# Optimization experiments

Measured on AMD Instinct MI355X. Metric: run time of the kernel, lower is better.

Reference implementation:

```python
import jax, jax.numpy as jnp
import numpy as np

IN_CH = 512; OUT_CH = 512; NOISE_SIZE = 512; K = 3; A = 0.2
B = 4; H = 32
_G = float(np.sqrt(2.0 / (1.0 + A * A)))                 # leaky_relu gain, a=0.2
CONV_SCALE = _G / float(np.sqrt(IN_CH * K * K))          # equal-lr kaiming scale (fan_in = in_ch*3*3)
MS_SCALE = float(np.sqrt(2.0 / (NOISE_SIZE + IN_CH)))    # equal-lr xavier scale on make_s linear
RGB_SCALE = _G * float(np.sqrt(2.0 / (OUT_CH + 3)))      # equal-lr xavier scale on 1x1 to_rgb


def upsample2x(x):
    # torch F.interpolate(scale_factor=2, mode='bilinear', align_corners=False)
    b, c, h, w = x.shape
    return jax.image.resize(x, (b, c, 2 * h, 2 * w), method='bilinear')


def mod_conv(x, style, weight, bias, ms_w, ms_b, w_scale, demodulate, pad):
    # style -> per-sample input-channel scales s: (B, Cin)
    s = style @ (ms_w.T * MS_SCALE) + ms_b
    Wmod = (weight * w_scale)[None] * s[:, None, :, None, None]   # (B, Cout, Cin, k, k)
    if demodulate:
        d = jax.lax.rsqrt(jnp.sum(Wmod * Wmod, axis=(2, 3, 4)) + 1e-8)
        Wmod = Wmod * d[:, :, None, None, None]
    conv1 = lambda xi, wi: jax.lax.conv_general_dilated(
        xi[None], wi, (1, 1), [(pad, pad), (pad, pad)],
        dimension_numbers=('NCHW', 'OIHW', 'NCHW'))[0]
    y = jax.vmap(conv1)(x, Wmod)                                   # per-sample weights == grouped conv
    return y + bias[None, :, None, None]


def lrelu(x):
    return jnp.where(x >= 0, x, A * x)


def setup_inputs() -> dict:
    key = jax.random.key(0)
    ks = jax.random.split(key, 19)
    r = lambda i, shape: jax.random.normal(ks[i], shape, dtype=jnp.float32)
    return {
        'maps': r(0, (B, IN_CH, H, H)),
        'w': r(1, (B, NOISE_SIZE)),
        'rgb': r(2, (B, 3, H, H)),
        'noise0': r(3, (B, 1, 2 * H, 2 * H)),
        'noise1': r(4, (B, 1, 2 * H, 2 * H)),
        'conv0_w': r(5, (OUT_CH, IN_CH, K, K)),
        'conv0_b': 0.1 * r(6, (OUT_CH,)),
        'ms0_w': r(7, (IN_CH, NOISE_SIZE)),
        'ms0_b': jnp.ones((IN_CH,), jnp.float32),
        'ns0': 0.1 * r(8, (OUT_CH,)),
        'conv1_w': r(9, (OUT_CH, OUT_CH, K, K)),
        'conv1_b': 0.1 * r(10, (OUT_CH,)),
        'ms1_w': r(11, (OUT_CH, NOISE_SIZE)),
        'ms1_b': jnp.ones((OUT_CH,), jnp.float32),
        'ns1': 0.1 * r(12, (OUT_CH,)),
        'rgb_w': r(13, (3, OUT_CH, 1, 1)),
        'rgb_b': 0.1 * r(14, (3,)),
        'msr_w': r(15, (OUT_CH, NOISE_SIZE)),
        'msr_b': jnp.ones((OUT_CH,), jnp.float32),
    }


def reference(maps, w, rgb, noise0, noise1,
              conv0_w, conv0_b, ms0_w, ms0_b, ns0,
              conv1_w, conv1_b, ms1_w, ms1_b, ns1,
              rgb_w, rgb_b, msr_w, msr_b):
    # upsample branch (upsample=True)
    rgb = upsample2x(rgb)
    maps = upsample2x(maps)
    # layer 0: modulated conv -> noise -> leaky relu
    h = mod_conv(maps, w, conv0_w, conv0_b, ms0_w, ms0_b, CONV_SCALE, True, 1)
    h = lrelu(h + ns0[None, :, None, None] * noise0)
    # layer 1
    h = mod_conv(h, w, conv1_w, conv1_b, ms1_w, ms1_b, CONV_SCALE, True, 1)
    h = lrelu(h + ns1[None, :, None, None] * noise1)
    # to_rgb: 1x1 modulated conv, no demodulation
    rgb_out = rgb + mod_conv(h, w, rgb_w, rgb_b, msr_w, msr_b, RGB_SCALE, False, 0)
    return (rgb_out, h)
```

## Files before the change

### kernel.cpp

```cpp
#include <hip/hip_runtime.h>
#include <stdint.h>


#define BATCH 4
#define CH 512
#define NPP 4356
#define HOUT_OFF 49152

static constexpr double G_GAIN = 1.3867504905630728;
static constexpr float CONV_SCALE_F = (float)(G_GAIN / 67.88225099390857);
static constexpr float MS_SCALE_F = 0.044194173824159216f;
static constexpr float RGB_SCALE_F = (float)(G_GAIN * 1.4142135623730951 / 22.693611435820433);

typedef __attribute__((ext_vector_type(8))) short short8;
typedef __attribute__((ext_vector_type(4))) float floatx4;

#define OFF_S0     256
#define OFF_S1     (OFF_S0 + 8192)
#define OFF_SR     (OFF_S1 + 8192)
#define OFF_D0     (OFF_SR + 8192)
#define OFF_D1     (OFF_D0 + 8192)
#define OFF_B0F    (OFF_D1 + 8192)
#define OFF_B1F    (OFF_B0F + 2048)
#define OFF_NS0F   (OFF_B1F + 2048)
#define OFF_NS1F   (OFF_NS0F + 2048)
#define OFF_WMODR  (OFF_NS1F + 2048)
#define OFF_N0F    (OFF_WMODR + 24576)
#define OFF_N1F    (OFF_N0F + 65536)
#define OFF_WT0    (OFF_N1F + 65536)
#define WT_BYTES   4718592
#define OFF_WT1    (OFF_WT0 + WT_BYTES)
#define OFF_XP0    (OFF_WT1 + WT_BYTES)
#define XP_BYTES   17842176
#define OFF_XP1    (OFF_XP0 + XP_BYTES)

__device__ __forceinline__ float bf2f(unsigned short u) {
  return __uint_as_float(((unsigned int)u) << 16);
}
__device__ __forceinline__ unsigned short f2bf(float f) {
  unsigned int x = __float_as_uint(f);
  unsigned int r = x + 0x7FFFu + ((x >> 16) & 1u);
  return (unsigned short)(r >> 16);
}
__device__ __forceinline__ float ldin(const void* p, long i, int bf) {
  if (bf) return bf2f(((const unsigned short*)p)[i]);
  return ((const float*)p)[i];
}
__device__ __forceinline__ int bfflag_of(const void* msb) {
  return ((const unsigned int*)msb)[0] == 0x3F803F80u ? 1 : 0;
}
__device__ __forceinline__ void async_ld16(const void* g, void* l) {
  __builtin_amdgcn_global_load_lds(
      (const __attribute__((address_space(1))) unsigned int*)g,
      (__attribute__((address_space(3))) unsigned int*)l, 16, 0, 0);
}
__device__ __forceinline__ void upw(int o, int n_in, int& lo, int& hi, float& wlo) {
  int k = o >> 1;
  if (o & 1) { lo = k; hi = k + 1; if (hi > n_in - 1) hi = n_in - 1; wlo = 0.75f; }
  else       { lo = k - 1; if (lo < 0) lo = 0; hi = k; wlo = 0.25f; }
}

__global__ void k_pre(const void* w, const void* msw0, const void* msb0,
                      const void* msw1, const void* msb1,
                      const void* mswr, const void* msbr,
                      const void* b0, const void* b1, const void* nv0,
                      const void* nv1, const void* noise0, const void* noise1,
                      float* s0, float* s1, float* sr,
                      float* ob0, float* ob1, float* ons0, float* ons1,
                      float* on0, float* on1, unsigned short* Xp) {
  const int bf = bfflag_of(msb0);
  const int bid = blockIdx.x;
  if (bid < 264) {
    const int idx = bid * 256 + threadIdx.x;
    const int plane = idx / 132;
    const int rem = idx - plane * 132;
    const int row65 = rem >= 66;
    const int col = rem - (row65 ? 66 : 0);
    const short8 z = {0, 0, 0, 0, 0, 0, 0, 0};
    *(short8*)&Xp[((long)plane * NPP + (row65 ? 65 : 0) * 66 + col) * 8] = z;
    return;
  }
  if (bid < 648) {
    const int b2 = bid - 264;
    const int mat = b2 >> 7, chunk = b2 & 127;
    const int wv = threadIdx.x >> 6, lane = threadIdx.x & 63;
    const int i = chunk * 4 + wv;
    const void* msw; const void* msb; float* out;
    if (mat == 0)      { msw = msw0; msb = msb0; out = s0; }
    else if (mat == 1) { msw = msw1; msb = msb1; out = s1; }
    else               { msw = mswr; msb = msbr; out = sr; }
    float a[4] = {0.f, 0.f, 0.f, 0.f};
    const int n0 = lane * 8;
    if (bf) {
      short8 m8 = *(const short8*)((const unsigned short*)msw + (long)i * 512 + n0);
      for (int b = 0; b < 4; ++b) {
        short8 w8 = *(const short8*)((const unsigned short*)w + b * 512 + n0);
        float s = 0.f;
        for (int e = 0; e < 8; ++e)
          s += bf2f((unsigned short)m8[e]) * bf2f((unsigned short)w8[e]);
        a[b] = s;
      }
    } else {
      const float* mrow = (const float*)msw + (long)i * 512 + n0;
      float4 m0v = *(const float4*)mrow, m1v = *(const float4*)(mrow + 4);
      for (int b = 0; b < 4; ++b) {
        const float* wr = (const float*)w + b * 512 + n0;
        float4 w0v = *(const float4*)wr, w1v = *(const float4*)(wr + 4);
        a[b] = m0v.x * w0v.x + m0v.y * w0v.y + m0v.z * w0v.z + m0v.w * w0v.w +
               m1v.x * w1v.x + m1v.y * w1v.y + m1v.z * w1v.z + m1v.w * w1v.w;
      }
    }
    for (int off = 1; off < 64; off <<= 1)
      for (int b = 0; b < 4; ++b) a[b] += __shfl_xor(a[b], off, 64);
    if (lane == 0) {
      const float mb = ldin(msb, i, bf);
      for (int b = 0; b < 4; ++b) out[b * 512 + i] = a[b] * MS_SCALE_F + mb;
    }
    return;
  }
  const int t = (bid - 648) * 256 + threadIdx.x;
  if (t < 512) {
    ob0[t] = ldin(b0, t, bf); ob1[t] = ldin(b1, t, bf);
    ons0[t] = ldin(nv0, t, bf); ons1[t] = ldin(nv1, t, bf);
  }
  on0[t] = ldin(noise0, t, bf);
  on1[t] = ldin(noise1, t, bf);
}

__global__ void k_mid(const void* w0, const void* w1,
                      const float* s0, const float* s1, const float* sr,
                      const void* rw, unsigned short* Wt0, unsigned short* Wt1,
                      float* S0, float* S1, float* owmr,
                      const void* maps, unsigned short* Xp0, const void* msb) {
  const int bf = bfflag_of(msb);
  const int bid = blockIdx.x;
  __shared__ float smem[32 * 4 * 32];
  if (bid < 256) {
    const int l = bid >> 7, cog = bid & 127;
    const void* w = l ? w1 : w0;
    const float* s = l ? s1 : s0;
    unsigned short* Wt = l ? Wt1 : Wt0;
    float* S = l ? S1 : S0;
    const int co_sub = threadIdx.x >> 6;
    const int kb = (threadIdx.x >> 2) & 15, q = threadIdx.x & 3;
    const int co = cog * 4 + co_sub;
    const int ci0 = kb * 32 + q * 8;
    const long base = ((long)co * 512 + ci0) * 9;
    float v[9][8];
    if (bf) {
      const unsigned short* wp = (const unsigned short*)w + base;
      short8 r[9];
#pragma unroll
      for (int k = 0; k < 9; ++k) r[k] = *(const short8*)(wp + k * 8);
#pragma unroll
      for (int j = 0; j < 8; ++j)
#pragma unroll
        for (int t = 0; t < 9; ++t) {
          const int off = j * 9 + t;
          v[t][j] = bf2f((unsigned short)r[off >> 3][off & 7]);
        }
    } else {
      const float* wp = (const float*)w + base;
      float4 r[18];
#pragma unroll
      for (int k = 0; k < 18; ++k) r[k] = *(const float4*)(wp + k * 4);
#pragma unroll
      for (int j = 0; j < 8; ++j)
#pragma unroll
        for (int t = 0; t < 9; ++t) {
          const int off = j * 9 + t;
          const float4 rr = r[off >> 2];
          const int c2 = off & 3;
          v[t][j] = c2 == 0 ? rr.x : (c2 == 1 ? rr.y : (c2 == 2 ? rr.z : rr.w));
        }
    }
#pragma unroll
    for (int t = 0; t < 9; ++t) {
      short8 pk;
#pragma unroll
      for (int j = 0; j < 8; ++j) pk[j] = (short)f2bf(v[t][j]);
      *(short8*)&Wt[((long)(t * 16 + kb) * 4 + q) * 4096 + co * 8] = pk;
    }
    float wsq[8];
#pragma unroll
    for (int j = 0; j < 8; ++j) {
      float a = 0.f;
#pragma unroll
      for (int t = 0; t < 9; ++t) a += v[t][j] * v[t][j];
      wsq[j] = a;
    }
    float part[4];
#pragma unroll
    for (int b4 = 0; b4 < 4; ++b4) {
      const float* sp = s + b4 * 512 + ci0;
      float4 sa = *(const float4*)sp, sb = *(const float4*)(sp + 4);
      part[b4] = sa.x * sa.x * wsq[0] + sa.y * sa.y * wsq[1] +
                 sa.z * sa.z * wsq[2] + sa.w * sa.w * wsq[3] +
                 sb.x * sb.x * wsq[4] + sb.y * sb.y * wsq[5] +
                 sb.z * sb.z * wsq[6] + sb.w * sb.w * wsq[7];
    }
    for (int off = 1; off < 64; off <<= 1)
#pragma unroll
      for (int b4 = 0; b4 < 4; ++b4)
        part[b4] += __shfl_xor(part[b4], off, 64);
    if ((threadIdx.x & 63) == 0)
#pragma unroll
      for (int b4 = 0; b4 < 4; ++b4) S[b4 * 512 + co] = part[b4];
    return;
  }
  if (bid < 1280) {
    const int bid2 = bid - 256;
    const int t = bid2 & 15, kb = (bid2 >> 4) & 15, b = bid2 >> 8;
    float (*lds)[4][32] = (float(*)[4][32])smem;
    {
      const int ciq = threadIdx.x >> 5;
      const int x = threadIdx.x & 31;
      for (int cc = 0; cc < 4; ++cc) {
        const int ci = cc * 8 + ciq;
        const long cbase = ((long)(b * 512 + kb * 32 + ci)) << 10;
        for (int r = 0; r < 4; ++r) {
          int ir = 2 * t - 1 + r;
          ir = ir < 0 ? 0 : (ir > 31 ? 31 : ir);
          lds[ci][r][x] = ldin(maps, cbase + ir * 32 + x, bf);
        }
      }
    }
    __syncthreads();
    const int q = threadIdx.x >> 6, px = threadIdx.x & 63;
    int xlo, xhi; float wx;
    upw(px, 32, xlo, xhi, wx);
    float sv[8];
    for (int jj = 0; jj < 8; ++jj) sv[jj] = s0[b * 512 + kb * 32 + q * 8 + jj];
    for (int y = 0; y < 4; ++y) {
      const int yg = 4 * t + y;
      int ylo, yhi; float wy;
      upw(yg, 32, ylo, yhi, wy);
      const int rlo = ylo - (2 * t - 1), rhi = yhi - (2 * t - 1);
      short8 pk;
      for (int jj = 0; jj < 8; ++jj) {
        const int ci = q * 8 + jj;
        float vlo = wx * lds[ci][rlo][xlo] + (1.f - wx) * lds[ci][rlo][xhi];
        float vhi = wx * lds[ci][rhi][xlo] + (1.f - wx) * lds[ci][rhi][xhi];
        float v = (wy * vlo + (1.f - wy) * vhi) * sv[jj];
        pk[jj] = (short)f2bf(v);
      }
      *(short8*)&Xp0[((((long)b * 16 + kb) * 4 + q) * NPP + (yg + 1) * 66 + (px + 1)) * 8] = pk;
    }
    return;
  }
  const int i = (bid - 1280) * 256 + threadIdx.x;
  const int b = i / 1536; const int r = i - b * 1536;
  const int c = r >> 9; const int ci = r & 511;
  owmr[i] = RGB_SCALE_F * ldin(rw, c * 512 + ci, bf) * sr[b * 512 + ci];
}

#define MFMA16 __builtin_amdgcn_mfma_f32_16x16x32_bf16
template <int LAYER>
__global__ __launch_bounds__(512, 2) void k_conv(
    const unsigned short* __restrict__ Wt,
    const unsigned short* Xp,
    const float* __restrict__ Ssum,
    const float* __restrict__ bias,
    const float* __restrict__ nsc,
    const float* __restrict__ noise,
    const float* __restrict__ snext,
    unsigned short* XpOut,
    void* dout,
    const void* __restrict__ msb) {
  __shared__ __align__(16) unsigned short AB[49152];
  const int idx = blockIdx.x;
  const int mt = idx & 3, b = (idx >> 2) & 3, nt = idx >> 4;
  const int m0 = mt << 7, y0 = nt << 2;
  const int lane = threadIdx.x & 63, wv = threadIdx.x >> 6;
  const int wm = wv >> 2, wn = wv & 3;
  const int q = lane >> 4, l15 = lane & 15;

  const floatx4 vz = {0.f, 0.f, 0.f, 0.f};
  floatx4 c00 = vz, c01 = vz, c02 = vz, c03 = vz;
  floatx4 c10 = vz, c11 = vz, c12 = vz, c13 = vz;
  floatx4 c20 = vz, c21 = vz, c22 = vz, c23 = vz;
  floatx4 c30 = vz, c31 = vz, c32 = vz, c33 = vz;

  const int vA = (q << 10) + (wm << 9) + (l15 << 3);
  const int BB = 24576;
  const int vB   = (q << 9) + (l15 << 3);
  const int vBm1 = (q << 9) + ((l15 == 0 ? 0 : l15 - 1) << 3);
  const int vBp1 = (q << 9) + ((l15 == 15 ? 15 : l15 + 1) << 3);
  const bool e0 = (l15 == 0), e15 = (l15 == 15);

  auto issueB6 = [&](int kbn, int half) {
#pragma unroll
    for (int k = 0; k < 3; ++k) {
      const int t = wv * 3 + k;
      const int row = t >> 2, qq = t & 3;
      const unsigned short* src =
          Xp + ((((long)b * 16 + kbn) * 4 + qq) * NPP + (long)(y0 + row) * 66 + 1 + lane) * 8;
      async_ld16(src, &AB[BB + half * 12288 + ((row * 4 + qq) << 9)]);
    }
  };
  auto issueA = [&](int kb, int ky, int par) {
#pragma unroll
    for (int k = 0; k < 3; ++k) {
      const int c = wv * 3 + k;
      const int half64 = c & 1, chunk = c >> 1;
      const int kx = chunk >> 2, qq = chunk & 3;
      const unsigned short* src =
          Wt + ((long)(((ky * 3 + kx) * 16 + kb) * 4 + qq) << 12) +
          ((m0 + half64 * 64 + lane) << 3);
      async_ld16(src, &AB[par * 12288 + chunk * 1024 + half64 * 512]);
    }
  };

  const short8 z8 = {0, 0, 0, 0, 0, 0, 0, 0};

#define RND(KY, PA, HB, KB, NKB, NKY, NPA, DOB, DKB, DHB)                      \
  {                                                                            \
    __syncthreads();                                                           \
    issueA((NKB), (NKY), (NPA));                                               \
    if (DOB) issueB6((DKB), (DHB));                                            \
    const int ab = (PA) * 12288 + vA;                                          \
    short8 a00 = *(const short8*)&AB[ab];                                      \
    short8 a01 = *(const short8*)&AB[ab + 128];                                \
    short8 a02 = *(const short8*)&AB[ab + 256];                                \
    short8 a03 = *(const short8*)&AB[ab + 384];                                \
    short8 a10 = *(const short8*)&AB[ab + 4096];                               \
    short8 a11 = *(const short8*)&AB[ab + 4224];                               \
    short8 a12 = *(const short8*)&AB[ab + 4352];                               \
    short8 a13 = *(const short8*)&AB[ab + 4480];                               \
    short8 a20 = *(const short8*)&AB[ab + 8192];                               \
    short8 a21 = *(const short8*)&AB[ab + 8320];                               \
    short8 a22 = *(const short8*)&AB[ab + 8448];                               \
    short8 a23 = *(const short8*)&AB[ab + 8576];                               \
    const int bo = BB + (HB) * 12288 + ((wn + (KY)) << 11);                    \
    {                                                              \
      short8 b0 = *(const short8*)&AB[vBm1 + bo];                              \
      short8 b1 = *(const short8*)&AB[vB + bo + 120];                          \
      short8 b2 = *(const short8*)&AB[vB + bo + 248];                          \
      short8 b3 = *(const short8*)&AB[vB + bo + 376];                          \
      b0 = e0 ? z8 : b0;                                                       \
      c00 = MFMA16(a00, b0, c00, 0, 0, 0); c01 = MFMA16(a00, b1, c01, 0, 0, 0);\
      c02 = MFMA16(a00, b2, c02, 0, 0, 0); c03 = MFMA16(a00, b3, c03, 0, 0, 0);\
      c10 = MFMA16(a01, b0, c10, 0, 0, 0); c11 = MFMA16(a01, b1, c11, 0, 0, 0);\
      c12 = MFMA16(a01, b2, c12, 0, 0, 0); c13 = MFMA16(a01, b3, c13, 0, 0, 0);\
      c20 = MFMA16(a02, b0, c20, 0, 0, 0); c21 = MFMA16(a02, b1, c21, 0, 0, 0);\
      c22 = MFMA16(a02, b2, c22, 0, 0, 0); c23 = MFMA16(a02, b3, c23, 0, 0, 0);\
      c30 = MFMA16(a03, b0, c30, 0, 0, 0); c31 = MFMA16(a03, b1, c31, 0, 0, 0);\
      c32 = MFMA16(a03, b2, c32, 0, 0, 0); c33 = MFMA16(a03, b3, c33, 0, 0, 0);\
    }                                                                          \
    {                                                              \
      short8 b0 = *(const short8*)&AB[vB + bo];                                \
      short8 b1 = *(const short8*)&AB[vB + bo + 128];                          \
      short8 b2 = *(const short8*)&AB[vB + bo + 256];                          \
      short8 b3 = *(const short8*)&AB[vB + bo + 384];                          \
      c00 = MFMA16(a10, b0, c00, 0, 0, 0); c01 = MFMA16(a10, b1, c01, 0, 0, 0);\
      c02 = MFMA16(a10, b2, c02, 0, 0, 0); c03 = MFMA16(a10, b3, c03, 0, 0, 0);\
      c10 = MFMA16(a11, b0, c10, 0, 0, 0); c11 = MFMA16(a11, b1, c11, 0, 0, 0);\
      c12 = MFMA16(a11, b2, c12, 0, 0, 0); c13 = MFMA16(a11, b3, c13, 0, 0, 0);\
      c20 = MFMA16(a12, b0, c20, 0, 0, 0); c21 = MFMA16(a12, b1, c21, 0, 0, 0);\
      c22 = MFMA16(a12, b2, c22, 0, 0, 0); c23 = MFMA16(a12, b3, c23, 0, 0, 0);\
      c30 = MFMA16(a13, b0, c30, 0, 0, 0); c31 = MFMA16(a13, b1, c31, 0, 0, 0);\
      c32 = MFMA16(a13, b2, c32, 0, 0, 0); c33 = MFMA16(a13, b3, c33, 0, 0, 0);\
    }                                                                          \
    {                                                              \
      short8 b0 = *(const short8*)&AB[vB + bo + 8];                            \
      short8 b1 = *(const short8*)&AB[vB + bo + 136];                          \
      short8 b2 = *(const short8*)&AB[vB + bo + 264];                          \
      short8 b3 = *(const short8*)&AB[vBp1 + bo + 384];                        \
      b3 = e15 ? z8 : b3;                                                      \
      c00 = MFMA16(a20, b0, c00, 0, 0, 0); c01 = MFMA16(a20, b1, c01, 0, 0, 0);\
      c02 = MFMA16(a20, b2, c02, 0, 0, 0); c03 = MFMA16(a20, b3, c03, 0, 0, 0);\
      c10 = MFMA16(a21, b0, c10, 0, 0, 0); c11 = MFMA16(a21, b1, c11, 0, 0, 0);\
      c12 = MFMA16(a21, b2, c12, 0, 0, 0); c13 = MFMA16(a21, b3, c13, 0, 0, 0);\
      c20 = MFMA16(a22, b0, c20, 0, 0, 0); c21 = MFMA16(a22, b1, c21, 0, 0, 0);\
      c22 = MFMA16(a22, b2, c22, 0, 0, 0); c23 = MFMA16(a22, b3, c23, 0, 0, 0);\
      c30 = MFMA16(a23, b0, c30, 0, 0, 0); c31 = MFMA16(a23, b1, c31, 0, 0, 0);\
      c32 = MFMA16(a23, b2, c32, 0, 0, 0); c33 = MFMA16(a23, b3, c33, 0, 0, 0);\
    }                                                                          \
  }

  issueA(0, 0, 0);
  issueB6(0, 0);

#pragma unroll 1
  for (int it = 0; it < 8; ++it) {
    const int kb = it * 2, kb1 = kb + 1, kb2 = (kb + 2) & 15;
    RND(0, 0, 0, kb,  kb,  1, 1, 1, kb1, 1)
    RND(1, 1, 0, kb,  kb,  2, 0, 0, 0,  0)
    RND(2, 0, 0, kb,  kb1, 0, 1, 0, 0,  0)
    RND(0, 1, 1, kb1, kb1, 1, 0, 1, kb2, 0)
    RND(1, 0, 1, kb1, kb1, 2, 1, 0, 0,  0)
    RND(2, 1, 1, kb1, kb2, 0, 0, 0, 0,  0)
  }
#undef RND

  floatx4 accv[4][4] = {{c00, c01, c02, c03}, {c10, c11, c12, c13},
                        {c20, c21, c22, c23}, {c30, c31, c32, c33}};
  const int bfflag = bfflag_of(msb);
  const int coB = m0 + (wm << 6) + ((lane >> 4) << 2);
  const int xB = lane & 15;
  const int y = y0 + wn;
  for (int i = 0; i < 4; ++i) {
    const int co = coB + (i << 4);
    float Ds[4], bi[4], nv[4], sx[4];
    for (int r = 0; r < 4; ++r) {
      float Sv = Ssum[b * 512 + co + r];
      Ds[r] = CONV_SCALE_F * rsqrtf(CONV_SCALE_F * CONV_SCALE_F * Sv + 1e-8f);
      bi[r] = bias[co + r];
      nv[r] = nsc[co + r];
      sx[r] = (LAYER == 0) ? snext[b * 512 + co + r] : 0.f;
    }
    for (int j = 0; j < 4; ++j) {
      const int x = (j << 4) + xB;
      const int p = (y << 6) + x;
      const float nz = noise[b * 4096 + p];
      if (LAYER == 0) {
        unsigned long long pk = 0ull;
        for (int r = 0; r < 4; ++r) {
          float v = accv[i][j][r] * Ds[r] + bi[r] + nv[r] * nz;
          v = (v >= 0.f) ? v : 0.2f * v;
          pk |= (unsigned long long)f2bf(v * sx[r]) << (16 * r);
        }
        const int pp = (y + 1) * 66 + (x + 1);
        const long o = ((((long)b * 16 + (co >> 5)) * 4 + ((co >> 3) & 3)) * NPP + pp) * 8 + (co & 7);
        *(unsigned long long*)(XpOut + o) = pk;
      } else {
        for (int r = 0; r < 4; ++r) {
          float v = accv[i][j][r] * Ds[r] + bi[r] + nv[r] * nz;
          v = (v >= 0.f) ? v : 0.2f * v;
          const long o = (((long)(b * 512 + co + r)) << 12) + p;
          if (bfflag) ((unsigned short*)dout)[HOUT_OFF + o] = f2bf(v);
          else        ((float*)dout)[HOUT_OFF + o] = v;
        }
      }
    }
  }
}

__global__ void k_rgb(const void* rgb_in, const float* wmodr, const void* rb,
                      void* dout, const void* msb) {
  const int bf = bfflag_of(msb);
  const int b = blockIdx.y, p0 = blockIdx.x * 512;
  const int g = threadIdx.x >> 6, lane = threadIdx.x & 63;
  const int px = p0 + lane * 8;
  const char* hbytes = (const char*)dout + (long)HOUT_OFF * (bf ? 2 : 4);
  const float* wm = wmodr + b * 1536;
  float a0[8] = {}, a1[8] = {}, a2[8] = {};
  for (int ci = g * 128; ci < g * 128 + 128; ++ci) {
    const long o = (((long)(b * 512 + ci)) << 12) + px;
    float hv[8];
    if (bf) {
      short8 h8 = *(const short8*)((const unsigned short*)hbytes + o);
#pragma unroll
      for (int k = 0; k < 8; ++k) hv[k] = bf2f((unsigned short)h8[k]);
    } else {
      float4 f0 = *(const float4*)((const float*)hbytes + o);
      float4 f1 = *(const float4*)((const float*)hbytes + o + 4);
      hv[0] = f0.x; hv[1] = f0.y; hv[2] = f0.z; hv[3] = f0.w;
      hv[4] = f1.x; hv[5] = f1.y; hv[6] = f1.z; hv[7] = f1.w;
    }
    const float w0 = wm[ci], w1 = wm[512 + ci], w2 = wm[1024 + ci];
#pragma unroll
    for (int k = 0; k < 8; ++k) {
      a0[k] += w0 * hv[k]; a1[k] += w1 * hv[k]; a2[k] += w2 * hv[k];
    }
  }
  __shared__ float red[4][3][512];
#pragma unroll
  for (int k = 0; k < 8; ++k) {
    red[g][0][lane * 8 + k] = a0[k];
    red[g][1][lane * 8 + k] = a1[k];
    red[g][2][lane * 8 + k] = a2[k];
  }
  __syncthreads();
  for (int e = 0; e < 2; ++e) {
    const int pp = threadIdx.x * 2 + e;
    const int p = p0 + pp;
    const int y = p >> 6, x = p & 63;
    int ylo, yhi, xlo, xhi; float wy, wx;
    upw(y, 32, ylo, yhi, wy);
    upw(x, 32, xlo, xhi, wx);
    for (int c = 0; c < 3; ++c) {
      float s = red[0][c][pp] + red[1][c][pp] + red[2][c][pp] + red[3][c][pp];
      const long base = (long)(b * 3 + c) << 10;
      const float v00 = ldin(rgb_in, base + ylo * 32 + xlo, bf);
      const float v01 = ldin(rgb_in, base + ylo * 32 + xhi, bf);
      const float v10 = ldin(rgb_in, base + yhi * 32 + xlo, bf);
      const float v11 = ldin(rgb_in, base + yhi * 32 + xhi, bf);
      const float up = wy * (wx * v00 + (1.f - wx) * v01) +
                       (1.f - wy) * (wx * v10 + (1.f - wx) * v11);
      const float v = up + s + ldin(rb, c, bf);
      const long o = ((long)(b * 3 + c) << 12) + p;
      if (bf) ((unsigned short*)dout)[o] = f2bf(v);
      else    ((float*)dout)[o] = v;
    }
  }
}

extern "C" void kernel_launch(void* const* d_in, const int* in_sizes, int n_in,
                              void* d_out, int out_size, void* d_ws, size_t ws_size,
                              hipStream_t stream) {
  char* ws = (char*)d_ws;
  float* s0 = (float*)(ws + OFF_S0);
  float* s1 = (float*)(ws + OFF_S1);
  float* sr = (float*)(ws + OFF_SR);
  float* S0 = (float*)(ws + OFF_D0);
  float* S1 = (float*)(ws + OFF_D1);
  float* b0f = (float*)(ws + OFF_B0F);
  float* b1f = (float*)(ws + OFF_B1F);
  float* ns0f = (float*)(ws + OFF_NS0F);
  float* ns1f = (float*)(ws + OFF_NS1F);
  float* wmodr = (float*)(ws + OFF_WMODR);
  float* n0f = (float*)(ws + OFF_N0F);
  float* n1f = (float*)(ws + OFF_N1F);
  unsigned short* Wt0 = (unsigned short*)(ws + OFF_WT0);
  unsigned short* Wt1 = (unsigned short*)(ws + OFF_WT1);
  unsigned short* Xp0 = (unsigned short*)(ws + OFF_XP0);
  unsigned short* Xp1 = (unsigned short*)(ws + OFF_XP1);

  k_pre<<<712, 256, 0, stream>>>(d_in[1], d_in[7], d_in[8], d_in[12], d_in[13],
                                 d_in[17], d_in[18], d_in[6], d_in[11], d_in[9],
                                 d_in[14], d_in[3], d_in[4],
                                 s0, s1, sr, b0f, b1f, ns0f, ns1f, n0f, n1f, Xp0);
  k_mid<<<1304, 256, 0, stream>>>(d_in[5], d_in[10], s0, s1, sr, d_in[15],
                                  Wt0, Wt1, S0, S1, wmodr, d_in[0], Xp0, d_in[8]);
  k_conv<0><<<256, 512, 0, stream>>>(Wt0, Xp0, S0, b0f, ns0f, n0f, s1, Xp1,
                                     d_out, d_in[8]);
  k_conv<1><<<256, 512, 0, stream>>>(Wt1, Xp1, S1, b1f, ns1f, n1f, s1, Xp1,
                                     d_out, d_in[8]);
  k_rgb<<<dim3(8, 4), 256, 0, stream>>>(d_in[2], wmodr, d_in[16], d_out, d_in[8]);
  (void)in_sizes; (void)n_in; (void)out_size; (void)ws_size;
}
```

Baseline: 283.7 us.

## Switch conv kernel to 32x32x16 MFMA with 4-wave blocks

The implicit-GEMM conv kernel now uses 32x32x16 bf16 MFMA tiles instead of 16x16x32, and halves the block to 4 waves that each own a larger 64x128 output tile. Each wave loads more async chunks per stage, and the LDS fragment addressing, the edge masking for the horizontal taps and the epilogue mapping are rewritten for the 32-lane layout. The aim is fewer LDS fragment reads per MFMA and higher MFMA throughput per instruction. In exchange each wave holds more accumulator registers and fewer waves are resident to hide latency.

```diff
diff --git a/kernel.cpp b/kernel.cpp
--- a/kernel.cpp
+++ b/kernel.cpp
@@ -14,6 +14,7 @@
 
 typedef __attribute__((ext_vector_type(8))) short short8;
 typedef __attribute__((ext_vector_type(4))) float floatx4;
+typedef __attribute__((ext_vector_type(16))) float floatx16;
 
 #define OFF_S0     256
 #define OFF_S1     (OFF_S0 + 8192)
@@ -254,9 +255,9 @@
   owmr[i] = RGB_SCALE_F * ldin(rw, c * 512 + ci, bf) * sr[b * 512 + ci];
 }
 
-#define MFMA16 __builtin_amdgcn_mfma_f32_16x16x32_bf16
+#define MFMA32 __builtin_amdgcn_mfma_f32_32x32x16_bf16
 template <int LAYER>
-__global__ __launch_bounds__(512, 2) void k_conv(
+__global__ __launch_bounds__(256, 1) void k_conv(
     const unsigned short* __restrict__ Wt,
     const unsigned short* Xp,
     const float* __restrict__ Ssum,
@@ -272,26 +273,25 @@
   const int mt = idx & 3, b = (idx >> 2) & 3, nt = idx >> 4;
   const int m0 = mt << 7, y0 = nt << 2;
   const int lane = threadIdx.x & 63, wv = threadIdx.x >> 6;
-  const int wm = wv >> 2, wn = wv & 3;
-  const int q = lane >> 4, l15 = lane & 15;
-
-  const floatx4 vz = {0.f, 0.f, 0.f, 0.f};
-  floatx4 c00 = vz, c01 = vz, c02 = vz, c03 = vz;
-  floatx4 c10 = vz, c11 = vz, c12 = vz, c13 = vz;
-  floatx4 c20 = vz, c21 = vz, c22 = vz, c23 = vz;
-  floatx4 c30 = vz, c31 = vz, c32 = vz, c33 = vz;
-
-  const int vA = (q << 10) + (wm << 9) + (l15 << 3);
+  const int wm = wv >> 1, wn = wv & 1, wn2 = wn << 1;
+  const int l31 = lane & 31, hi = lane >> 5;
+
+  const floatx16 vz = {0.f, 0.f, 0.f, 0.f, 0.f, 0.f, 0.f, 0.f,
+                       0.f, 0.f, 0.f, 0.f, 0.f, 0.f, 0.f, 0.f};
+  floatx16 d00 = vz, d01 = vz, d02 = vz, d03 = vz;
+  floatx16 d10 = vz, d11 = vz, d12 = vz, d13 = vz;
+
+  const int vA32 = (hi << 10) + (wm << 9) + (l31 << 3);
   const int BB = 24576;
-  const int vB   = (q << 9) + (l15 << 3);
-  const int vBm1 = (q << 9) + ((l15 == 0 ? 0 : l15 - 1) << 3);
-  const int vBp1 = (q << 9) + ((l15 == 15 ? 15 : l15 + 1) << 3);
-  const bool e0 = (l15 == 0), e15 = (l15 == 15);
+  const int vB32   = (hi << 9) + (l31 << 3);
+  const int vB32m1 = (hi << 9) + ((l31 == 0 ? 0 : l31 - 1) << 3);
+  const int vB32p1 = (hi << 9) + ((l31 == 31 ? 31 : l31 + 1) << 3);
+  const bool ee0 = (l31 == 0), ee31 = (l31 == 31);
 
   auto issueB6 = [&](int kbn, int half) {
 #pragma unroll
-    for (int k = 0; k < 3; ++k) {
-      const int t = wv * 3 + k;
+    for (int k = 0; k < 6; ++k) {
+      const int t = wv * 6 + k;
       const int row = t >> 2, qq = t & 3;
       const unsigned short* src =
           Xp + ((((long)b * 16 + kbn) * 4 + qq) * NPP + (long)(y0 + row) * 66 + 1 + lane) * 8;
@@ -300,8 +300,8 @@
   };
   auto issueA = [&](int kb, int ky, int par) {
 #pragma unroll
-    for (int k = 0; k < 3; ++k) {
-      const int c = wv * 3 + k;
+    for (int k = 0; k < 6; ++k) {
+      const int c = wv * 6 + k;
       const int half64 = c & 1, chunk = c >> 1;
       const int kx = chunk >> 2, qq = chunk & 3;
       const unsigned short* src =
@@ -313,69 +313,48 @@
 
   const short8 z8 = {0, 0, 0, 0, 0, 0, 0, 0};
 
+#define KSTEP(KX, S)                                                           \
+  {                                                                            \
+    const int ka = ab + (((KX)*4 + 2*(S)) << 10);                              \
+    const int ks = (S) << 10;                                                  \
+    short8 a0 = *(const short8*)&AB[ka + vA32];                                \
+    short8 a1 = *(const short8*)&AB[ka + vA32 + 256];                          \
+    short8 b0, b1, b2, b3;                                                     \
+    if ((KX) == 0) {                                                           \
+      b0 = *(const short8*)&AB[bo0 + ks + vB32m1];                             \
+      b1 = *(const short8*)&AB[bo0 + ks + vB32 + 248];                         \
+      b2 = *(const short8*)&AB[bo1 + ks + vB32m1];                             \
+      b3 = *(const short8*)&AB[bo1 + ks + vB32 + 248];                         \
+      b0 = ee0 ? z8 : b0; b2 = ee0 ? z8 : b2;                                  \
+    } else if ((KX) == 1) {                                                    \
+      b0 = *(const short8*)&AB[bo0 + ks + vB32];                               \
+      b1 = *(const short8*)&AB[bo0 + ks + vB32 + 256];                         \
+      b2 = *(const short8*)&AB[bo1 + ks + vB32];                               \
+      b3 = *(const short8*)&AB[bo1 + ks + vB32 + 256];                         \
+    } else {                                                                   \
+      b0 = *(const short8*)&AB[bo0 + ks + vB32 + 8];                           \
+      b1 = *(const short8*)&AB[bo0 + ks + vB32p1 + 256];                       \
+      b2 = *(const short8*)&AB[bo1 + ks + vB32 + 8];                           \
+      b3 = *(const short8*)&AB[bo1 + ks + vB32p1 + 256];                       \
+      b1 = ee31 ? z8 : b1; b3 = ee31 ? z8 : b3;                                \
+    }                                                                          \
+    d00 = MFMA32(a0, b0, d00, 0, 0, 0); d01 = MFMA32(a0, b1, d01, 0, 0, 0);    \
+    d02 = MFMA32(a0, b2, d02, 0, 0, 0); d03 = MFMA32(a0, b3, d03, 0, 0, 0);    \
+    d10 = MFMA32(a1, b0, d10, 0, 0, 0); d11 = MFMA32(a1, b1, d11, 0, 0, 0);    \
+    d12 = MFMA32(a1, b2, d12, 0, 0, 0); d13 = MFMA32(a1, b3, d13, 0, 0, 0);    \
+  }
+
 #define RND(KY, PA, HB, KB, NKB, NKY, NPA, DOB, DKB, DHB)                      \
   {                                                                            \
     __syncthreads();                                                           \
     issueA((NKB), (NKY), (NPA));                                               \
     if (DOB) issueB6((DKB), (DHB));                                            \
-    const int ab = (PA) * 12288 + vA;                                          \
-    short8 a00 = *(const short8*)&AB[ab];                                      \
-    short8 a01 = *(const short8*)&AB[ab + 128];                                \
-    short8 a02 = *(const short8*)&AB[ab + 256];                                \
-    short8 a03 = *(const short8*)&AB[ab + 384];                                \
-    short8 a10 = *(const short8*)&AB[ab + 4096];                               \
-    short8 a11 = *(const short8*)&AB[ab + 4224];                               \
-    short8 a12 = *(const short8*)&AB[ab + 4352];                               \
-    short8 a13 = *(const short8*)&AB[ab + 4480];                               \
-    short8 a20 = *(const short8*)&AB[ab + 8192];                               \
-    short8 a21 = *(const short8*)&AB[ab + 8320];                               \
-    short8 a22 = *(const short8*)&AB[ab + 8448];                               \
-    short8 a23 = *(const short8*)&AB[ab + 8576];                               \
-    const int bo = BB + (HB) * 12288 + ((wn + (KY)) << 11);                    \
-    {                                                              \
-      short8 b0 = *(const short8*)&AB[vBm1 + bo];                              \
-      short8 b1 = *(const short8*)&AB[vB + bo + 120];                          \
-      short8 b2 = *(const short8*)&AB[vB + bo + 248];                          \
-      short8 b3 = *(const short8*)&AB[vB + bo + 376];                          \
-      b0 = e0 ? z8 : b0;                                                       \
-      c00 = MFMA16(a00, b0, c00, 0, 0, 0); c01 = MFMA16(a00, b1, c01, 0, 0, 0);\
-      c02 = MFMA16(a00, b2, c02, 0, 0, 0); c03 = MFMA16(a00, b3, c03, 0, 0, 0);\
-      c10 = MFMA16(a01, b0, c10, 0, 0, 0); c11 = MFMA16(a01, b1, c11, 0, 0, 0);\
-      c12 = MFMA16(a01, b2, c12, 0, 0, 0); c13 = MFMA16(a01, b3, c13, 0, 0, 0);\
-      c20 = MFMA16(a02, b0, c20, 0, 0, 0); c21 = MFMA16(a02, b1, c21, 0, 0, 0);\
-      c22 = MFMA16(a02, b2, c22, 0, 0, 0); c23 = MFMA16(a02, b3, c23, 0, 0, 0);\
-      c30 = MFMA16(a03, b0, c30, 0, 0, 0); c31 = MFMA16(a03, b1, c31, 0, 0, 0);\
-      c32 = MFMA16(a03, b2, c32, 0, 0, 0); c33 = MFMA16(a03, b3, c33, 0, 0, 0);\
-    }                                                                          \
-    {                                                              \
-      short8 b0 = *(const short8*)&AB[vB + bo];                                \
-      short8 b1 = *(const short8*)&AB[vB + bo + 128];                          \
-      short8 b2 = *(const short8*)&AB[vB + bo + 256];                          \
-      short8 b3 = *(const short8*)&AB[vB + bo + 384];                          \
-      c00 = MFMA16(a10, b0, c00, 0, 0, 0); c01 = MFMA16(a10, b1, c01, 0, 0, 0);\
-      c02 = MFMA16(a10, b2, c02, 0, 0, 0); c03 = MFMA16(a10, b3, c03, 0, 0, 0);\
-      c10 = MFMA16(a11, b0, c10, 0, 0, 0); c11 = MFMA16(a11, b1, c11, 0, 0, 0);\
-      c12 = MFMA16(a11, b2, c12, 0, 0, 0); c13 = MFMA16(a11, b3, c13, 0, 0, 0);\
-      c20 = MFMA16(a12, b0, c20, 0, 0, 0); c21 = MFMA16(a12, b1, c21, 0, 0, 0);\
-      c22 = MFMA16(a12, b2, c22, 0, 0, 0); c23 = MFMA16(a12, b3, c23, 0, 0, 0);\
-      c30 = MFMA16(a13, b0, c30, 0, 0, 0); c31 = MFMA16(a13, b1, c31, 0, 0, 0);\
-      c32 = MFMA16(a13, b2, c32, 0, 0, 0); c33 = MFMA16(a13, b3, c33, 0, 0, 0);\
-    }                                                                          \
-    {                                                              \
-      short8 b0 = *(const short8*)&AB[vB + bo + 8];                            \
-      short8 b1 = *(const short8*)&AB[vB + bo + 136];                          \
-      short8 b2 = *(const short8*)&AB[vB + bo + 264];                          \
-      short8 b3 = *(const short8*)&AB[vBp1 + bo + 384];                        \
-      b3 = e15 ? z8 : b3;                                                      \
-      c00 = MFMA16(a20, b0, c00, 0, 0, 0); c01 = MFMA16(a20, b1, c01, 0, 0, 0);\
-      c02 = MFMA16(a20, b2, c02, 0, 0, 0); c03 = MFMA16(a20, b3, c03, 0, 0, 0);\
-      c10 = MFMA16(a21, b0, c10, 0, 0, 0); c11 = MFMA16(a21, b1, c11, 0, 0, 0);\
-      c12 = MFMA16(a21, b2, c12, 0, 0, 0); c13 = MFMA16(a21, b3, c13, 0, 0, 0);\
-      c20 = MFMA16(a22, b0, c20, 0, 0, 0); c21 = MFMA16(a22, b1, c21, 0, 0, 0);\
-      c22 = MFMA16(a22, b2, c22, 0, 0, 0); c23 = MFMA16(a22, b3, c23, 0, 0, 0);\
-      c30 = MFMA16(a23, b0, c30, 0, 0, 0); c31 = MFMA16(a23, b1, c31, 0, 0, 0);\
-      c32 = MFMA16(a23, b2, c32, 0, 0, 0); c33 = MFMA16(a23, b3, c33, 0, 0, 0);\
-    }                                                                          \
+    const int ab = (PA) * 12288;                                               \
+    const int bo0 = BB + (HB) * 12288 + ((wn2 + (KY)) << 11);                  \
+    const int bo1 = bo0 + 2048;                                                \
+    KSTEP(0, 0) KSTEP(0, 1)                                                    \
+    KSTEP(1, 0) KSTEP(1, 1)                                                    \
+    KSTEP(2, 0) KSTEP(2, 1)                                                    \
   }
 
   issueA(0, 0, 0);
@@ -392,44 +371,51 @@
     RND(2, 1, 1, kb1, kb2, 0, 0, 0, 0,  0)
   }
 #undef RND
-
-  floatx4 accv[4][4] = {{c00, c01, c02, c03}, {c10, c11, c12, c13},
-                        {c20, c21, c22, c23}, {c30, c31, c32, c33}};
+#undef KSTEP
+
+  floatx16 accv[2][4] = {{d00, d01, d02, d03}, {d10, d11, d12, d13}};
   const int bfflag = bfflag_of(msb);
-  const int coB = m0 + (wm << 6) + ((lane >> 4) << 2);
-  const int xB = lane & 15;
-  const int y = y0 + wn;
-  for (int i = 0; i < 4; ++i) {
-    const int co = coB + (i << 4);
-    float Ds[4], bi[4], nv[4], sx[4];
-    for (int r = 0; r < 4; ++r) {
-      float Sv = Ssum[b * 512 + co + r];
-      Ds[r] = CONV_SCALE_F * rsqrtf(CONV_SCALE_F * CONV_SCALE_F * Sv + 1e-8f);
-      bi[r] = bias[co + r];
-      nv[r] = nsc[co + r];
-      sx[r] = (LAYER == 0) ? snext[b * 512 + co + r] : 0.f;
-    }
-    for (int j = 0; j < 4; ++j) {
-      const int x = (j << 4) + xB;
-      const int p = (y << 6) + x;
-      const float nz = noise[b * 4096 + p];
-      if (LAYER == 0) {
-        unsigned long long pk = 0ull;
-        for (int r = 0; r < 4; ++r) {
-          float v = accv[i][j][r] * Ds[r] + bi[r] + nv[r] * nz;
-          v = (v >= 0.f) ? v : 0.2f * v;
-          pk |= (unsigned long long)f2bf(v * sx[r]) << (16 * r);
-        }
-        const int pp = (y + 1) * 66 + (x + 1);
-        const long o = ((((long)b * 16 + (co >> 5)) * 4 + ((co >> 3) & 3)) * NPP + pp) * 8 + (co & 7);
-        *(unsigned long long*)(XpOut + o) = pk;
-      } else {
-        for (int r = 0; r < 4; ++r) {
-          float v = accv[i][j][r] * Ds[r] + bi[r] + nv[r] * nz;
-          v = (v >= 0.f) ? v : 0.2f * v;
-          const long o = (((long)(b * 512 + co + r)) << 12) + p;
-          if (bfflag) ((unsigned short*)dout)[HOUT_OFF + o] = f2bf(v);
-          else        ((float*)dout)[HOUT_OFF + o] = v;
+  const int cb = m0 + (wm << 6);
+#pragma unroll
+  for (int i = 0; i < 2; ++i) {
+#pragma unroll
+    for (int g = 0; g < 4; ++g) {
+      const int cg = cb + i * 32 + g * 8 + 4 * hi;
+      float Ds[4], bi[4], nv[4], sx[4];
+#pragma unroll
+      for (int r = 0; r < 4; ++r) {
+        float Sv = Ssum[b * 512 + cg + r];
+        Ds[r] = CONV_SCALE_F * rsqrtf(CONV_SCALE_F * CONV_SCALE_F * Sv + 1e-8f);
+        bi[r] = bias[cg + r];
+        nv[r] = nsc[cg + r];
+        sx[r] = (LAYER == 0) ? snext[b * 512 + cg + r] : 0.f;
+      }
+#pragma unroll
+      for (int j = 0; j < 4; ++j) {
+        const int y = y0 + wn2 + (j >> 1);
+        const int x = ((j & 1) << 5) + l31;
+        const int p = (y << 6) + x;
+        const float nz = noise[b * 4096 + p];
+        if (LAYER == 0) {
+          unsigned long long pk = 0ull;
+#pragma unroll
+          for (int r = 0; r < 4; ++r) {
+            float v = accv[i][j][g * 4 + r] * Ds[r] + bi[r] + nv[r] * nz;
+            v = (v >= 0.f) ? v : 0.2f * v;
+            pk |= (unsigned long long)f2bf(v * sx[r]) << (16 * r);
+          }
+          const int pp = (y + 1) * 66 + (x + 1);
+          const long o = ((((long)b * 16 + (cg >> 5)) * 4 + ((cg >> 3) & 3)) * NPP + pp) * 8 + (cg & 7);
+          *(unsigned long long*)(XpOut + o) = pk;
+        } else {
+#pragma unroll
+          for (int r = 0; r < 4; ++r) {
+            float v = accv[i][j][g * 4 + r] * Ds[r] + bi[r] + nv[r] * nz;
+            v = (v >= 0.f) ? v : 0.2f * v;
+            const long o = (((long)(b * 512 + cg + r)) << 12) + p;
+            if (bfflag) ((unsigned short*)dout)[HOUT_OFF + o] = f2bf(v);
+            else        ((float*)dout)[HOUT_OFF + o] = v;
+          }
         }
       }
     }
@@ -523,9 +509,9 @@
                                  s0, s1, sr, b0f, b1f, ns0f, ns1f, n0f, n1f, Xp0);
   k_mid<<<1304, 256, 0, stream>>>(d_in[5], d_in[10], s0, s1, sr, d_in[15],
                                   Wt0, Wt1, S0, S1, wmodr, d_in[0], Xp0, d_in[8]);
-  k_conv<0><<<256, 512, 0, stream>>>(Wt0, Xp0, S0, b0f, ns0f, n0f, s1, Xp1,
+  k_conv<0><<<256, 256, 0, stream>>>(Wt0, Xp0, S0, b0f, ns0f, n0f, s1, Xp1,
                                      d_out, d_in[8]);
-  k_conv<1><<<256, 512, 0, stream>>>(Wt1, Xp1, S1, b1f, ns1f, n1f, s1, Xp1,
+  k_conv<1><<<256, 256, 0, stream>>>(Wt1, Xp1, S1, b1f, ns1f, n1f, s1, Xp1,
                                      d_out, d_in[8]);
   k_rgb<<<dim3(8, 4), 256, 0, stream>>>(d_in[2], wmodr, d_in[16], d_out, d_in[8]);
   (void)in_sizes; (void)n_in; (void)out_size; (void)ws_size;
```

New measurement: 306.4 us. +8.0%, slower.
